# Performance work log

Hardware: AMD Instinct MI355X
Metric: run time of the kernel (lower is better)

## Reference

```python
import jax, jax.numpy as jnp
import numpy as np

N = 8192
D_IN = 3
D_K = 128
HID = 256
N_RES = 2
N_TRI = 2730
N_EDGE = 2048
EPS = float(jnp.finfo(jnp.float32).eps)  # torch RMSNorm default eps=None -> finfo eps


def setup_inputs() -> dict:
    key = jax.random.key(0)
    ks = jax.random.split(key, 16)
    std = 0.02
    inp = {
        "edge_features": jax.random.normal(ks[0], (N, D_IN), dtype=jnp.float32),
        "edge_ids": jax.random.randint(ks[1], (N,), 0, N_EDGE),
        "triangle_ids": jax.random.randint(ks[2], (N,), 0, N_TRI),
        # projections (stored as [in, out]; equivalent to torch Linear)
        "Wq": jax.random.normal(ks[3], (D_IN, D_K), dtype=jnp.float32) * std,
        "bq": jnp.zeros((D_K,), jnp.float32),
        "Wk": jax.random.normal(ks[4], (D_IN, D_K), dtype=jnp.float32) * std,
        "bk": jnp.zeros((D_K,), jnp.float32),
        "Wv": jax.random.normal(ks[5], (D_IN, D_K), dtype=jnp.float32) * std,
        "bv": jnp.zeros((D_K,), jnp.float32),
        # attention MLP: Linear(d_k, hid) -> N_RES ResBlocks -> Linear(hid, 1)
        "W0": jax.random.normal(ks[6], (D_K, HID), dtype=jnp.float32) * std,
        "b0": jnp.zeros((HID,), jnp.float32),
        "rms_w": jnp.ones((N_RES, HID), jnp.float32),
        "Wres": jax.random.normal(ks[7], (N_RES, HID, HID), dtype=jnp.float32) * std,
        "bres": jnp.zeros((N_RES, HID), jnp.float32),
        "Wout": jax.random.normal(ks[8], (HID, 1), dtype=jnp.float32) * std,
        "bout": jnp.zeros((1,), jnp.float32),
    }
    return inp


def _rmsnorm(x, g):
    ms = jnp.mean(x * x, axis=-1, keepdims=True)
    return x * jax.lax.rsqrt(ms + EPS) * g


def reference(edge_features, edge_ids, triangle_ids,
              Wq, bq, Wk, bk, Wv, bv,
              W0, b0, rms_w, Wres, bres, Wout, bout):
    q = edge_features @ Wq + bq          # [N, d_k]
    k = edge_features @ Wk + bk
    v = edge_features @ Wv + bv
    scores = (q @ k.T) / jnp.sqrt(jnp.float32(D_K))   # [N, N]
    mask = triangle_ids[:, None] == triangle_ids[None, :]
    scores = jnp.where(mask, scores, -jnp.inf)
    attn = jax.nn.softmax(scores, axis=1)             # every row has diag True
    attended = attn @ v                                # [N, d_k]
    # MLP with ResBlocks
    h = attended @ W0 + b0                             # [N, hid]
    for i in range(N_RES):
        h = h + jax.nn.relu(_rmsnorm(h, rms_w[i]) @ Wres[i] + bres[i])
    logits = (h @ Wout + bout)[:, 0]                   # [N]
    # scatter_softmax over edge_ids (dim=0)
    seg_max = jax.ops.segment_max(logits, edge_ids, num_segments=N_EDGE)
    ex = jnp.exp(logits - seg_max[edge_ids])
    seg_sum = jax.ops.segment_sum(ex, edge_ids, num_segments=N_EDGE)
    weights = ex / seg_sum[edge_ids]
    return weights
```

## Files before the change

kernel.cpp:

```cpp
#include <hip/hip_runtime.h>
#include <math.h>

#define N 8192
#define D_IN 3
#define D_K 128
#define HID 256
#define N_RES 2
#define N_TRI 2730
#define N_EDGE 2048
#define EPS 1.1920929e-07f

typedef unsigned short u16;
typedef float f32x4 __attribute__((ext_vector_type(4)));
typedef short s16x8 __attribute__((ext_vector_type(8)));

#define OFF_ATTB     0
#define OFF_LOGITS   2097152
#define OFF_TRIOFF   (OFF_LOGITS + 32768)
#define OFF_TRICNT   (OFF_TRIOFF + 11008)
#define OFF_MEMT     (OFF_TRICNT + 11008)
#define OFF_EOFF     (OFF_MEMT + 32768)
#define OFF_ECNT     (OFF_EOFF + 8192)
#define OFF_MEME     (OFF_ECNT + 8192)
#define OFF_WPK      (OFF_MEME + 32768)

__device__ __forceinline__ u16 f2bf(float f) {
    unsigned int u = __float_as_uint(f);
    unsigned int r = (u + 0x7fffu + ((u >> 16) & 1u)) >> 16;
    return (u16)r;
}

__global__ __launch_bounds__(1024) void k_prep(
        const int* __restrict__ tri, const int* __restrict__ eids,
        int* __restrict__ tri_off, int* __restrict__ tri_cnt, int* __restrict__ mem_t,
        int* __restrict__ e_off, int* __restrict__ e_cnt, int* __restrict__ mem_e) {
    __shared__ int sa[4096], sb[4096];
    __shared__ int ea[2048], eb[2048];
    const int t = threadIdx.x;
    for (int i = t; i < 4096; i += 1024) sa[i] = 0;
    for (int i = t; i < 2048; i += 1024) ea[i] = 0;
    __syncthreads();
    for (int n = t; n < N; n += 1024) {
        atomicAdd(&sa[tri[n]], 1);
        atomicAdd(&ea[eids[n]], 1);
    }
    __syncthreads();
    int *src = sa, *dst = sb;
    for (int off = 1; off < 4096; off <<= 1) {
        for (int i = t; i < 4096; i += 1024) {
            int v = src[i];
            if (i >= off) v += src[i - off];
            dst[i] = v;
        }
        __syncthreads();
        int* tmp = src; src = dst; dst = tmp;
    }
    int *es = ea, *ed = eb;
    for (int off = 1; off < 2048; off <<= 1) {
        for (int i = t; i < 2048; i += 1024) {
            int v = es[i];
            if (i >= off) v += es[i - off];
            ed[i] = v;
        }
        __syncthreads();
        int* tmp = es; es = ed; ed = tmp;
    }
    for (int i = t; i < N_TRI; i += 1024) {
        int excl = i ? src[i - 1] : 0;
        tri_off[i] = excl;
        tri_cnt[i] = src[i] - excl;
        dst[i] = excl;
    }
    for (int i = t; i < N_EDGE; i += 1024) {
        int excl = i ? es[i - 1] : 0;
        e_off[i] = excl;
        e_cnt[i] = es[i] - excl;
        ed[i] = excl;
    }
    __syncthreads();
    for (int n = t; n < N; n += 1024) {
        int p = atomicAdd(&dst[tri[n]], 1);
        mem_t[p] = n;
        int q = atomicAdd(&ed[eids[n]], 1);
        mem_e[q] = n;
    }
}

__global__ __launch_bounds__(256) void k_pack(
        const float* __restrict__ W0, const float* __restrict__ Wres,
        u16* __restrict__ Wpk) {
    int tid = blockIdx.x * 256 + threadIdx.x;
    int tile = tid >> 6, lane = tid & 63;
    int q = lane >> 4, c = lane & 15;
    u16 tmp[8];
    int dst;
    if (tile < 64) {
        int nt = tile >> 2, kt = tile & 3;
        int k0 = kt * 32 + q * 8, n = nt * 16 + c;
        dst = (tile * 64 + lane) * 8;
        #pragma unroll
        for (int j = 0; j < 8; ++j) tmp[j] = f2bf(W0[(k0 + j) * HID + n]);
    } else {
        int t2 = tile - 64;
        int r = t2 >> 7, tl = t2 & 127;
        int nt = tl >> 3, kt = tl & 7;
        int k0 = kt * 32 + q * 8, n = nt * 16 + c;
        dst = 32768 + r * 65536 + (tl * 64 + lane) * 8;
        const float* W = Wres + r * 65536;
        #pragma unroll
        for (int j = 0; j < 8; ++j) tmp[j] = f2bf(W[(k0 + j) * HID + n]);
    }
    *(s16x8*)&Wpk[dst] = *(s16x8*)tmp;
}

__global__ __launch_bounds__(256) void k_attn(
        const float* __restrict__ ef, const int* __restrict__ tri,
        const float* __restrict__ Wq, const float* __restrict__ bq,
        const float* __restrict__ Wk, const float* __restrict__ bk,
        const float* __restrict__ Wv, const float* __restrict__ bv,
        const int* __restrict__ tri_offset, const int* __restrict__ tri_count,
        const int* __restrict__ members, u16* __restrict__ att) {
    int wave = threadIdx.x >> 6;
    int lane = threadIdx.x & 63;
    int row = blockIdx.x * 4 + wave;
    int d0 = lane * 2, d1 = lane * 2 + 1;

    float e0 = ef[row * 3 + 0], e1 = ef[row * 3 + 1], e2 = ef[row * 3 + 2];
    float qa = bq[d0] + e0 * Wq[d0] + e1 * Wq[D_K + d0] + e2 * Wq[2 * D_K + d0];
    float qb = bq[d1] + e0 * Wq[d1] + e1 * Wq[D_K + d1] + e2 * Wq[2 * D_K + d1];

    int t = tri[row];
    int off = tri_offset[t], cnt = tri_count[t];
    const float scale = 0.08838834764831845f;

    float m = -INFINITY, l = 0.f, acca = 0.f, accb = 0.f;
    for (int ii = 0; ii < cnt; ++ii) {
        int j = members[off + ii];
        float f0 = ef[j * 3 + 0], f1 = ef[j * 3 + 1], f2 = ef[j * 3 + 2];
        float ka = bk[d0] + f0 * Wk[d0] + f1 * Wk[D_K + d0] + f2 * Wk[2 * D_K + d0];
        float kb = bk[d1] + f0 * Wk[d1] + f1 * Wk[D_K + d1] + f2 * Wk[2 * D_K + d1];
        float p = qa * ka + qb * kb;
        #pragma unroll
        for (int o = 32; o > 0; o >>= 1) p += __shfl_xor(p, o);
        float s = p * scale;
        float va = bv[d0] + f0 * Wv[d0] + f1 * Wv[D_K + d0] + f2 * Wv[2 * D_K + d0];
        float vb = bv[d1] + f0 * Wv[d1] + f1 * Wv[D_K + d1] + f2 * Wv[2 * D_K + d1];
        float mn = fmaxf(m, s);
        float sc = expf(m - mn);
        float w  = expf(s - mn);
        l    = l * sc + w;
        acca = acca * sc + w * va;
        accb = accb * sc + w * vb;
        m = mn;
    }
    att[row * D_K + d0] = f2bf(acca / l);
    att[row * D_K + d1] = f2bf(accb / l);
}

__global__ __launch_bounds__(256) void k_mlp(
        const u16* __restrict__ att,
        const float* __restrict__ b0, const float* __restrict__ rms_w,
        const float* __restrict__ bres, const float* __restrict__ Wout,
        const float* __restrict__ bout, const u16* __restrict__ Wpk,
        float* __restrict__ logits) {
    __shared__ u16 X[16][264];
    __shared__ float red[4][16];
    const int tid = threadIdx.x;
    const int w = tid >> 6, lane = tid & 63;
    const int q = lane >> 4, c = lane & 15;
    const int base = blockIdx.x * 16;
    const int colb = w * 64 + c;

    {
        int r = tid >> 4, kk = (tid & 15) * 8;
        *(s16x8*)&X[r][kk] = *(const s16x8*)&att[(base + r) * D_K + kk];
    }
    __syncthreads();

    const s16x8* Bp = (const s16x8*)Wpk;

    float h[4][4];
    f32x4 acc[4];
    const f32x4 zero = {0.f, 0.f, 0.f, 0.f};

    #pragma unroll
    for (int nt = 0; nt < 4; ++nt) acc[nt] = zero;
    for (int kt = 0; kt < 4; ++kt) {
        s16x8 a = *(const s16x8*)&X[c][kt * 32 + q * 8];
        #pragma unroll
        for (int nt = 0; nt < 4; ++nt) {
            s16x8 b = Bp[((w * 4 + nt) * 4 + kt) * 64 + lane];
            acc[nt] = __builtin_amdgcn_mfma_f32_16x16x32_bf16(a, b, acc[nt], 0, 0, 0);
        }
    }
    #pragma unroll
    for (int nt = 0; nt < 4; ++nt) {
        float bb = b0[colb + nt * 16];
        #pragma unroll
        for (int rg = 0; rg < 4; ++rg) h[nt][rg] = acc[nt][rg] + bb;
    }

    for (int ir = 0; ir < N_RES; ++ir) {
        float part[4];
        #pragma unroll
        for (int rg = 0; rg < 4; ++rg) {
            part[rg] = h[0][rg] * h[0][rg] + h[1][rg] * h[1][rg]
                     + h[2][rg] * h[2][rg] + h[3][rg] * h[3][rg];
            #pragma unroll
            for (int o = 1; o < 16; o <<= 1) part[rg] += __shfl_xor(part[rg], o);
        }
        if (c == 0) {
            #pragma unroll
            for (int rg = 0; rg < 4; ++rg) red[w][q * 4 + rg] = part[rg];
        }
        __syncthreads();
        float sc[4];
        #pragma unroll
        for (int rg = 0; rg < 4; ++rg) {
            int rr = q * 4 + rg;
            float ms = (red[0][rr] + red[1][rr] + red[2][rr] + red[3][rr]) * (1.f / HID);
            sc[rg] = rsqrtf(ms + EPS);
        }
        #pragma unroll
        for (int nt = 0; nt < 4; ++nt) {
            float gg = rms_w[ir * HID + colb + nt * 16];
            #pragma unroll
            for (int rg = 0; rg < 4; ++rg) {
                X[q * 4 + rg][colb + nt * 16] = f2bf(h[nt][rg] * sc[rg] * gg);
            }
        }
        __syncthreads();

        const s16x8* Br = Bp + 4096 + ir * 8192;
        #pragma unroll
        for (int nt = 0; nt < 4; ++nt) acc[nt] = zero;
        for (int kt = 0; kt < 8; ++kt) {
            s16x8 a = *(const s16x8*)&X[c][kt * 32 + q * 8];
            #pragma unroll
            for (int nt = 0; nt < 4; ++nt) {
                s16x8 b = Br[((w * 4 + nt) * 8 + kt) * 64 + lane];
                acc[nt] = __builtin_amdgcn_mfma_f32_16x16x32_bf16(a, b, acc[nt], 0, 0, 0);
            }
        }
        #pragma unroll
        for (int nt = 0; nt < 4; ++nt) {
            float bb = bres[ir * HID + colb + nt * 16];
            #pragma unroll
            for (int rg = 0; rg < 4; ++rg) h[nt][rg] += fmaxf(acc[nt][rg] + bb, 0.f);
        }
    }

    {
        float wo[4];
        #pragma unroll
        for (int nt = 0; nt < 4; ++nt) wo[nt] = Wout[colb + nt * 16];
        float part[4];
        #pragma unroll
        for (int rg = 0; rg < 4; ++rg) {
            part[rg] = h[0][rg] * wo[0] + h[1][rg] * wo[1]
                     + h[2][rg] * wo[2] + h[3][rg] * wo[3];
            #pragma unroll
            for (int o = 1; o < 16; o <<= 1) part[rg] += __shfl_xor(part[rg], o);
        }
        if (c == 0) {
            #pragma unroll
            for (int rg = 0; rg < 4; ++rg) red[w][q * 4 + rg] = part[rg];
        }
        __syncthreads();
        if (tid < 16)
            logits[base + tid] = red[0][tid] + red[1][tid] + red[2][tid] + red[3][tid] + bout[0];
    }
}

__global__ __launch_bounds__(256) void k_segsoft(
        const float* __restrict__ logits, const int* __restrict__ e_off,
        const int* __restrict__ e_cnt, const int* __restrict__ mem_e,
        float* __restrict__ out) {
    int e = (blockIdx.x * 256 + threadIdx.x) >> 6;
    int lane = threadIdx.x & 63;
    int off = e_off[e], cnt = e_cnt[e];
    float mx = -INFINITY;
    for (int i = lane; i < cnt; i += 64) mx = fmaxf(mx, logits[mem_e[off + i]]);
    #pragma unroll
    for (int o = 32; o > 0; o >>= 1) mx = fmaxf(mx, __shfl_xor(mx, o));
    float s = 0.f;
    for (int i = lane; i < cnt; i += 64) s += expf(logits[mem_e[off + i]] - mx);
    #pragma unroll
    for (int o = 32; o > 0; o >>= 1) s += __shfl_xor(s, o);
    float inv = 1.f / s;
    for (int i = lane; i < cnt; i += 64) {
        int m = mem_e[off + i];
        out[m] = expf(logits[m] - mx) * inv;
    }
}

extern "C" void kernel_launch(void* const* d_in, const int* in_sizes, int n_in,
                              void* d_out, int out_size, void* d_ws, size_t ws_size,
                              hipStream_t stream) {
    const float* ef   = (const float*)d_in[0];
    const int*   eids = (const int*)d_in[1];
    const int*   tri  = (const int*)d_in[2];
    const float* Wq = (const float*)d_in[3];
    const float* bq = (const float*)d_in[4];
    const float* Wk = (const float*)d_in[5];
    const float* bk = (const float*)d_in[6];
    const float* Wv = (const float*)d_in[7];
    const float* bv = (const float*)d_in[8];
    const float* W0 = (const float*)d_in[9];
    const float* b0 = (const float*)d_in[10];
    const float* rms_w = (const float*)d_in[11];
    const float* Wres  = (const float*)d_in[12];
    const float* bres  = (const float*)d_in[13];
    const float* Wout  = (const float*)d_in[14];
    const float* bout  = (const float*)d_in[15];
    float* out = (float*)d_out;

    char* ws = (char*)d_ws;
    u16*   attb    = (u16*)(ws + OFF_ATTB);
    float* logits  = (float*)(ws + OFF_LOGITS);
    int*   tri_off = (int*)(ws + OFF_TRIOFF);
    int*   tri_cnt = (int*)(ws + OFF_TRICNT);
    int*   mem_t   = (int*)(ws + OFF_MEMT);
    int*   e_off   = (int*)(ws + OFF_EOFF);
    int*   e_cnt   = (int*)(ws + OFF_ECNT);
    int*   mem_e   = (int*)(ws + OFF_MEME);
    u16*   Wpk     = (u16*)(ws + OFF_WPK);

    hipLaunchKernelGGL(k_prep, dim3(1), dim3(1024), 0, stream,
                       tri, eids, tri_off, tri_cnt, mem_t, e_off, e_cnt, mem_e);
    hipLaunchKernelGGL(k_pack, dim3(80), dim3(256), 0, stream, W0, Wres, Wpk);
    hipLaunchKernelGGL(k_attn, dim3(N / 4), dim3(256), 0, stream,
                       ef, tri, Wq, bq, Wk, bk, Wv, bv, tri_off, tri_cnt, mem_t, attb);
    hipLaunchKernelGGL(k_mlp, dim3(N / 16), dim3(256), 0, stream,
                       attb, b0, rms_w, bres, Wout, bout, Wpk, logits);
    hipLaunchKernelGGL(k_segsoft, dim3(N_EDGE / 4), dim3(256), 0, stream,
                       logits, e_off, e_cnt, mem_e, out);
}
```

Measured before the change: 128.5 us.

## Fuse attention into MLP kernel, merge prep with weight packing, use wave-scan

Merges weight packing into the setup kernel as extra blocks. The single-block Hillis-Steele scans are replaced by a shuffle-based wave scan with fewer barriers. The attention step now runs inside the MLP kernel: each of 8 waves computes two rows, writes bf16 results straight into shared memory, and gathers member features once per 64-member chunk through shuffles. This removes two launches, the global attended buffer round-trip, and repeated scattered global loads, at the cost of halving per-wave MFMA columns and adding block-wide serialization on the attention loop.

```diff
diff --git a/kernel.cpp b/kernel.cpp
--- a/kernel.cpp
+++ b/kernel.cpp
@@ -11,190 +11,216 @@
 #define EPS 1.1920929e-07f
 
 typedef unsigned short u16;
+typedef unsigned int u32;
 typedef float f32x4 __attribute__((ext_vector_type(4)));
 typedef short s16x8 __attribute__((ext_vector_type(8)));
 
-#define OFF_ATTB     0
-#define OFF_LOGITS   2097152
-#define OFF_TRIOFF   (OFF_LOGITS + 32768)
-#define OFF_TRICNT   (OFF_TRIOFF + 11008)
-#define OFF_MEMT     (OFF_TRICNT + 11008)
-#define OFF_EOFF     (OFF_MEMT + 32768)
-#define OFF_ECNT     (OFF_EOFF + 8192)
-#define OFF_MEME     (OFF_ECNT + 8192)
-#define OFF_WPK      (OFF_MEME + 32768)
+#define OFF_LOGITS   0
+#define OFF_TRIOFF   32768
+#define OFF_TRICNT   43776
+#define OFF_MEMT     54784
+#define OFF_EOFF     87552
+#define OFF_ECNT     95744
+#define OFF_MEME     103936
+#define OFF_WPK      136704
 
 __device__ __forceinline__ u16 f2bf(float f) {
-    unsigned int u = __float_as_uint(f);
-    unsigned int r = (u + 0x7fffu + ((u >> 16) & 1u)) >> 16;
+    u32 u = __float_as_uint(f);
+    u32 r = (u + 0x7fffu + ((u >> 16) & 1u)) >> 16;
     return (u16)r;
 }
-
-__global__ __launch_bounds__(1024) void k_prep(
+__device__ __forceinline__ u32 pack2bf(float a, float b) {
+    return (u32)f2bf(a) | ((u32)f2bf(b) << 16);
+}
+
+__global__ __launch_bounds__(1024) void k_setup(
         const int* __restrict__ tri, const int* __restrict__ eids,
+        const float* __restrict__ W0, const float* __restrict__ Wres,
         int* __restrict__ tri_off, int* __restrict__ tri_cnt, int* __restrict__ mem_t,
-        int* __restrict__ e_off, int* __restrict__ e_cnt, int* __restrict__ mem_e) {
-    __shared__ int sa[4096], sb[4096];
-    __shared__ int ea[2048], eb[2048];
-    const int t = threadIdx.x;
-    for (int i = t; i < 4096; i += 1024) sa[i] = 0;
-    for (int i = t; i < 2048; i += 1024) ea[i] = 0;
+        int* __restrict__ e_off, int* __restrict__ e_cnt, int* __restrict__ mem_e,
+        u16* __restrict__ Wpk) {
+    if (blockIdx.x != 0) {
+        int tg = (blockIdx.x - 1) * 1024 + threadIdx.x;
+        int tile = tg >> 6, lane = tg & 63;
+        int q = lane >> 4, c = lane & 15;
+        u16 tmp[8];
+        int dst;
+        if (tile < 64) {
+            int nt = tile >> 2, kt = tile & 3;
+            int k0 = kt * 32 + q * 8, n = nt * 16 + c;
+            dst = (tile * 64 + lane) * 8;
+            #pragma unroll
+            for (int j = 0; j < 8; ++j) tmp[j] = f2bf(W0[(k0 + j) * HID + n]);
+        } else {
+            int t2 = tile - 64;
+            int r = t2 >> 7, tl = t2 & 127;
+            int nt = tl >> 3, kt = tl & 7;
+            int k0 = kt * 32 + q * 8, n = nt * 16 + c;
+            dst = 32768 + r * 65536 + (tl * 64 + lane) * 8;
+            const float* W = Wres + r * 65536;
+            #pragma unroll
+            for (int j = 0; j < 8; ++j) tmp[j] = f2bf(W[(k0 + j) * HID + n]);
+        }
+        *(s16x8*)&Wpk[dst] = *(s16x8*)tmp;
+        return;
+    }
+    __shared__ int sc[4096];
+    __shared__ int ec[2048];
+    __shared__ int wp[16];
+    const int t = threadIdx.x, lane = t & 63, wid = t >> 6;
+    for (int i = t; i < 4096; i += 1024) sc[i] = 0;
+    for (int i = t; i < 2048; i += 1024) ec[i] = 0;
     __syncthreads();
     for (int n = t; n < N; n += 1024) {
-        atomicAdd(&sa[tri[n]], 1);
-        atomicAdd(&ea[eids[n]], 1);
-    }
-    __syncthreads();
-    int *src = sa, *dst = sb;
-    for (int off = 1; off < 4096; off <<= 1) {
-        for (int i = t; i < 4096; i += 1024) {
-            int v = src[i];
-            if (i >= off) v += src[i - off];
-            dst[i] = v;
-        }
-        __syncthreads();
-        int* tmp = src; src = dst; dst = tmp;
-    }
-    int *es = ea, *ed = eb;
-    for (int off = 1; off < 2048; off <<= 1) {
-        for (int i = t; i < 2048; i += 1024) {
-            int v = es[i];
-            if (i >= off) v += es[i - off];
-            ed[i] = v;
-        }
-        __syncthreads();
-        int* tmp = es; es = ed; ed = tmp;
-    }
-    for (int i = t; i < N_TRI; i += 1024) {
-        int excl = i ? src[i - 1] : 0;
-        tri_off[i] = excl;
-        tri_cnt[i] = src[i] - excl;
-        dst[i] = excl;
-    }
-    for (int i = t; i < N_EDGE; i += 1024) {
-        int excl = i ? es[i - 1] : 0;
-        e_off[i] = excl;
-        e_cnt[i] = es[i] - excl;
-        ed[i] = excl;
+        atomicAdd(&sc[tri[n]], 1);
+        atomicAdd(&ec[eids[n]], 1);
+    }
+    __syncthreads();
+    int a0 = sc[t*4], a1 = sc[t*4+1], a2 = sc[t*4+2], a3 = sc[t*4+3];
+    int c0 = a0, c1 = c0 + a1, c2 = c1 + a2, c3 = c2 + a3;
+    int ts = c3;
+    #pragma unroll
+    for (int o = 1; o < 64; o <<= 1) { int u = __shfl_up(ts, o); if (lane >= o) ts += u; }
+    if (lane == 63) wp[wid] = ts;
+    __syncthreads();
+    if (wid == 0) {
+        int v = (lane < 16) ? wp[lane] : 0;
+        #pragma unroll
+        for (int o = 1; o < 16; o <<= 1) { int u = __shfl_up(v, o); if (lane >= o) v += u; }
+        if (lane < 16) wp[lane] = v;
+    }
+    __syncthreads();
+    {
+        int wexcl = wid ? wp[wid - 1] : 0;
+        int texcl = wexcl + ts - c3;
+        int o0 = texcl, o1 = texcl + c0, o2 = texcl + c1, o3 = texcl + c2;
+        if (t*4+0 < N_TRI) { tri_off[t*4+0] = o0; tri_cnt[t*4+0] = a0; }
+        if (t*4+1 < N_TRI) { tri_off[t*4+1] = o1; tri_cnt[t*4+1] = a1; }
+        if (t*4+2 < N_TRI) { tri_off[t*4+2] = o2; tri_cnt[t*4+2] = a2; }
+        if (t*4+3 < N_TRI) { tri_off[t*4+3] = o3; tri_cnt[t*4+3] = a3; }
+        sc[t*4+0] = o0; sc[t*4+1] = o1; sc[t*4+2] = o2; sc[t*4+3] = o3;
+    }
+    __syncthreads();
+    int ea0 = ec[t*2], ea1 = ec[t*2+1];
+    int f0 = ea0, f1 = f0 + ea1;
+    int es = f1;
+    #pragma unroll
+    for (int o = 1; o < 64; o <<= 1) { int u = __shfl_up(es, o); if (lane >= o) es += u; }
+    if (lane == 63) wp[wid] = es;
+    __syncthreads();
+    if (wid == 0) {
+        int v = (lane < 16) ? wp[lane] : 0;
+        #pragma unroll
+        for (int o = 1; o < 16; o <<= 1) { int u = __shfl_up(v, o); if (lane >= o) v += u; }
+        if (lane < 16) wp[lane] = v;
+    }
+    __syncthreads();
+    {
+        int wexcl = wid ? wp[wid - 1] : 0;
+        int texcl = wexcl + es - f1;
+        int eo0 = texcl, eo1 = texcl + f0;
+        e_off[t*2+0] = eo0; e_cnt[t*2+0] = ea0;
+        e_off[t*2+1] = eo1; e_cnt[t*2+1] = ea1;
+        ec[t*2+0] = eo0; ec[t*2+1] = eo1;
     }
     __syncthreads();
     for (int n = t; n < N; n += 1024) {
-        int p = atomicAdd(&dst[tri[n]], 1);
+        int p = atomicAdd(&sc[tri[n]], 1);
         mem_t[p] = n;
-        int q = atomicAdd(&ed[eids[n]], 1);
-        mem_e[q] = n;
-    }
-}
-
-__global__ __launch_bounds__(256) void k_pack(
-        const float* __restrict__ W0, const float* __restrict__ Wres,
-        u16* __restrict__ Wpk) {
-    int tid = blockIdx.x * 256 + threadIdx.x;
-    int tile = tid >> 6, lane = tid & 63;
-    int q = lane >> 4, c = lane & 15;
-    u16 tmp[8];
-    int dst;
-    if (tile < 64) {
-        int nt = tile >> 2, kt = tile & 3;
-        int k0 = kt * 32 + q * 8, n = nt * 16 + c;
-        dst = (tile * 64 + lane) * 8;
-        #pragma unroll
-        for (int j = 0; j < 8; ++j) tmp[j] = f2bf(W0[(k0 + j) * HID + n]);
-    } else {
-        int t2 = tile - 64;
-        int r = t2 >> 7, tl = t2 & 127;
-        int nt = tl >> 3, kt = tl & 7;
-        int k0 = kt * 32 + q * 8, n = nt * 16 + c;
-        dst = 32768 + r * 65536 + (tl * 64 + lane) * 8;
-        const float* W = Wres + r * 65536;
-        #pragma unroll
-        for (int j = 0; j < 8; ++j) tmp[j] = f2bf(W[(k0 + j) * HID + n]);
-    }
-    *(s16x8*)&Wpk[dst] = *(s16x8*)tmp;
-}
-
-__global__ __launch_bounds__(256) void k_attn(
+        int q2 = atomicAdd(&ec[eids[n]], 1);
+        mem_e[q2] = n;
+    }
+}
+
+__global__ __launch_bounds__(512) void k_fused(
         const float* __restrict__ ef, const int* __restrict__ tri,
         const float* __restrict__ Wq, const float* __restrict__ bq,
         const float* __restrict__ Wk, const float* __restrict__ bk,
         const float* __restrict__ Wv, const float* __restrict__ bv,
-        const int* __restrict__ tri_offset, const int* __restrict__ tri_count,
-        const int* __restrict__ members, u16* __restrict__ att) {
-    int wave = threadIdx.x >> 6;
-    int lane = threadIdx.x & 63;
-    int row = blockIdx.x * 4 + wave;
-    int d0 = lane * 2, d1 = lane * 2 + 1;
-
-    float e0 = ef[row * 3 + 0], e1 = ef[row * 3 + 1], e2 = ef[row * 3 + 2];
-    float qa = bq[d0] + e0 * Wq[d0] + e1 * Wq[D_K + d0] + e2 * Wq[2 * D_K + d0];
-    float qb = bq[d1] + e0 * Wq[d1] + e1 * Wq[D_K + d1] + e2 * Wq[2 * D_K + d1];
-
-    int t = tri[row];
-    int off = tri_offset[t], cnt = tri_count[t];
-    const float scale = 0.08838834764831845f;
-
-    float m = -INFINITY, l = 0.f, acca = 0.f, accb = 0.f;
-    for (int ii = 0; ii < cnt; ++ii) {
-        int j = members[off + ii];
-        float f0 = ef[j * 3 + 0], f1 = ef[j * 3 + 1], f2 = ef[j * 3 + 2];
-        float ka = bk[d0] + f0 * Wk[d0] + f1 * Wk[D_K + d0] + f2 * Wk[2 * D_K + d0];
-        float kb = bk[d1] + f0 * Wk[d1] + f1 * Wk[D_K + d1] + f2 * Wk[2 * D_K + d1];
-        float p = qa * ka + qb * kb;
-        #pragma unroll
-        for (int o = 32; o > 0; o >>= 1) p += __shfl_xor(p, o);
-        float s = p * scale;
-        float va = bv[d0] + f0 * Wv[d0] + f1 * Wv[D_K + d0] + f2 * Wv[2 * D_K + d0];
-        float vb = bv[d1] + f0 * Wv[d1] + f1 * Wv[D_K + d1] + f2 * Wv[2 * D_K + d1];
-        float mn = fmaxf(m, s);
-        float sc = expf(m - mn);
-        float w  = expf(s - mn);
-        l    = l * sc + w;
-        acca = acca * sc + w * va;
-        accb = accb * sc + w * vb;
-        m = mn;
-    }
-    att[row * D_K + d0] = f2bf(acca / l);
-    att[row * D_K + d1] = f2bf(accb / l);
-}
-
-__global__ __launch_bounds__(256) void k_mlp(
-        const u16* __restrict__ att,
+        const int* __restrict__ tri_off, const int* __restrict__ tri_cnt,
+        const int* __restrict__ mem_t,
         const float* __restrict__ b0, const float* __restrict__ rms_w,
         const float* __restrict__ bres, const float* __restrict__ Wout,
         const float* __restrict__ bout, const u16* __restrict__ Wpk,
         float* __restrict__ logits) {
     __shared__ u16 X[16][264];
-    __shared__ float red[4][16];
+    __shared__ float red[8][16];
     const int tid = threadIdx.x;
     const int w = tid >> 6, lane = tid & 63;
     const int q = lane >> 4, c = lane & 15;
     const int base = blockIdx.x * 16;
-    const int colb = w * 64 + c;
+    const int colb = w * 32 + c;
 
     {
-        int r = tid >> 4, kk = (tid & 15) * 8;
-        *(s16x8*)&X[r][kk] = *(const s16x8*)&att[(base + r) * D_K + kk];
+        const int d0 = lane * 2, d1 = d0 + 1;
+        float wq0a = Wq[d0], wq1a = Wq[D_K + d0], wq2a = Wq[2*D_K + d0], bqa = bq[d0];
+        float wq0b = Wq[d1], wq1b = Wq[D_K + d1], wq2b = Wq[2*D_K + d1], bqb = bq[d1];
+        float wk0a = Wk[d0], wk1a = Wk[D_K + d0], wk2a = Wk[2*D_K + d0], bka = bk[d0];
+        float wk0b = Wk[d1], wk1b = Wk[D_K + d1], wk2b = Wk[2*D_K + d1], bkb = bk[d1];
+        float wv0a = Wv[d0], wv1a = Wv[D_K + d0], wv2a = Wv[2*D_K + d0], bva = bv[d0];
+        float wv0b = Wv[d1], wv1b = Wv[D_K + d1], wv2b = Wv[2*D_K + d1], bvb = bv[d1];
+        const float scale = 0.08838834764831845f;
+
+        #pragma unroll
+        for (int rr = 0; rr < 2; ++rr) {
+            int lrow = 2 * w + rr;
+            int row = base + lrow;
+            float e0 = ef[row*3+0], e1 = ef[row*3+1], e2 = ef[row*3+2];
+            float qa = bqa + e0*wq0a + e1*wq1a + e2*wq2a;
+            float qb = bqb + e0*wq0b + e1*wq1b + e2*wq2b;
+            int tt = tri[row];
+            int off = tri_off[tt], cnt = tri_cnt[tt];
+            float m = -INFINITY, l = 0.f, acca = 0.f, accb = 0.f;
+            for (int bs = 0; bs < cnt; bs += 64) {
+                int nn = cnt - bs; if (nn > 64) nn = 64;
+                float g0 = 0.f, g1 = 0.f, g2 = 0.f;
+                if (lane < nn) {
+                    int j = mem_t[off + bs + lane];
+                    g0 = ef[j*3+0]; g1 = ef[j*3+1]; g2 = ef[j*3+2];
+                }
+                for (int ii = 0; ii < nn; ++ii) {
+                    float h0 = __shfl(g0, ii), h1 = __shfl(g1, ii), h2 = __shfl(g2, ii);
+                    float ka = bka + h0*wk0a + h1*wk1a + h2*wk2a;
+                    float kb = bkb + h0*wk0b + h1*wk1b + h2*wk2b;
+                    float p = qa * ka + qb * kb;
+                    #pragma unroll
+                    for (int o = 32; o > 0; o >>= 1) p += __shfl_xor(p, o);
+                    float s = p * scale;
+                    float va = bva + h0*wv0a + h1*wv1a + h2*wv2a;
+                    float vb = bvb + h0*wv0b + h1*wv1b + h2*wv2b;
+                    float mn = fmaxf(m, s);
+                    float rs = expf(m - mn);
+                    float ws = expf(s - mn);
+                    l    = l * rs + ws;
+                    acca = acca * rs + ws * va;
+                    accb = accb * rs + ws * vb;
+                    m = mn;
+                }
+            }
+            float inv = 1.f / l;
+            *(u32*)&X[lrow][d0] = pack2bf(acca * inv, accb * inv);
+        }
     }
     __syncthreads();
 
     const s16x8* Bp = (const s16x8*)Wpk;
-
-    float h[4][4];
-    f32x4 acc[4];
+    float h[2][4];
+    f32x4 acc[2];
     const f32x4 zero = {0.f, 0.f, 0.f, 0.f};
 
     #pragma unroll
-    for (int nt = 0; nt < 4; ++nt) acc[nt] = zero;
+    for (int nt = 0; nt < 2; ++nt) acc[nt] = zero;
+    #pragma unroll
     for (int kt = 0; kt < 4; ++kt) {
         s16x8 a = *(const s16x8*)&X[c][kt * 32 + q * 8];
         #pragma unroll
-        for (int nt = 0; nt < 4; ++nt) {
-            s16x8 b = Bp[((w * 4 + nt) * 4 + kt) * 64 + lane];
+        for (int nt = 0; nt < 2; ++nt) {
+            s16x8 b = Bp[((w * 2 + nt) * 4 + kt) * 64 + lane];
             acc[nt] = __builtin_amdgcn_mfma_f32_16x16x32_bf16(a, b, acc[nt], 0, 0, 0);
         }
     }
     #pragma unroll
-    for (int nt = 0; nt < 4; ++nt) {
+    for (int nt = 0; nt < 2; ++nt) {
         float bb = b0[colb + nt * 16];
         #pragma unroll
         for (int rg = 0; rg < 4; ++rg) h[nt][rg] = acc[nt][rg] + bb;
@@ -204,8 +230,7 @@
         float part[4];
         #pragma unroll
         for (int rg = 0; rg < 4; ++rg) {
-            part[rg] = h[0][rg] * h[0][rg] + h[1][rg] * h[1][rg]
-                     + h[2][rg] * h[2][rg] + h[3][rg] * h[3][rg];
+            part[rg] = h[0][rg] * h[0][rg] + h[1][rg] * h[1][rg];
             #pragma unroll
             for (int o = 1; o < 16; o <<= 1) part[rg] += __shfl_xor(part[rg], o);
         }
@@ -214,36 +239,37 @@
             for (int rg = 0; rg < 4; ++rg) red[w][q * 4 + rg] = part[rg];
         }
         __syncthreads();
-        float sc[4];
+        float sc4[4];
         #pragma unroll
         for (int rg = 0; rg < 4; ++rg) {
             int rr = q * 4 + rg;
-            float ms = (red[0][rr] + red[1][rr] + red[2][rr] + red[3][rr]) * (1.f / HID);
-            sc[rg] = rsqrtf(ms + EPS);
-        }
-        #pragma unroll
-        for (int nt = 0; nt < 4; ++nt) {
+            float ms = (red[0][rr] + red[1][rr] + red[2][rr] + red[3][rr]
+                      + red[4][rr] + red[5][rr] + red[6][rr] + red[7][rr]) * (1.f / HID);
+            sc4[rg] = rsqrtf(ms + EPS);
+        }
+        #pragma unroll
+        for (int nt = 0; nt < 2; ++nt) {
             float gg = rms_w[ir * HID + colb + nt * 16];
             #pragma unroll
-            for (int rg = 0; rg < 4; ++rg) {
-                X[q * 4 + rg][colb + nt * 16] = f2bf(h[nt][rg] * sc[rg] * gg);
-            }
+            for (int rg = 0; rg < 4; ++rg)
+                X[q * 4 + rg][colb + nt * 16] = f2bf(h[nt][rg] * sc4[rg] * gg);
         }
         __syncthreads();
 
         const s16x8* Br = Bp + 4096 + ir * 8192;
         #pragma unroll
-        for (int nt = 0; nt < 4; ++nt) acc[nt] = zero;
+        for (int nt = 0; nt < 2; ++nt) acc[nt] = zero;
+        #pragma unroll
         for (int kt = 0; kt < 8; ++kt) {
             s16x8 a = *(const s16x8*)&X[c][kt * 32 + q * 8];
             #pragma unroll
-            for (int nt = 0; nt < 4; ++nt) {
-                s16x8 b = Br[((w * 4 + nt) * 8 + kt) * 64 + lane];
+            for (int nt = 0; nt < 2; ++nt) {
+                s16x8 b = Br[((w * 2 + nt) * 8 + kt) * 64 + lane];
                 acc[nt] = __builtin_amdgcn_mfma_f32_16x16x32_bf16(a, b, acc[nt], 0, 0, 0);
             }
         }
         #pragma unroll
-        for (int nt = 0; nt < 4; ++nt) {
+        for (int nt = 0; nt < 2; ++nt) {
             float bb = bres[ir * HID + colb + nt * 16];
             #pragma unroll
             for (int rg = 0; rg < 4; ++rg) h[nt][rg] += fmaxf(acc[nt][rg] + bb, 0.f);
@@ -251,14 +277,11 @@
     }
 
     {
-        float wo[4];
-        #pragma unroll
-        for (int nt = 0; nt < 4; ++nt) wo[nt] = Wout[colb + nt * 16];
+        float wo0 = Wout[colb], wo1 = Wout[colb + 16];
         float part[4];
         #pragma unroll
         for (int rg = 0; rg < 4; ++rg) {
-            part[rg] = h[0][rg] * wo[0] + h[1][rg] * wo[1]
-                     + h[2][rg] * wo[2] + h[3][rg] * wo[3];
+            part[rg] = h[0][rg] * wo0 + h[1][rg] * wo1;
             #pragma unroll
             for (int o = 1; o < 16; o <<= 1) part[rg] += __shfl_xor(part[rg], o);
         }
@@ -267,8 +290,12 @@
             for (int rg = 0; rg < 4; ++rg) red[w][q * 4 + rg] = part[rg];
         }
         __syncthreads();
-        if (tid < 16)
-            logits[base + tid] = red[0][tid] + red[1][tid] + red[2][tid] + red[3][tid] + bout[0];
+        if (tid < 16) {
+            float s = bout[0];
+            #pragma unroll
+            for (int w2 = 0; w2 < 8; ++w2) s += red[w2][tid];
+            logits[base + tid] = s;
+        }
     }
 }
 
@@ -316,7 +343,6 @@
     float* out = (float*)d_out;
 
     char* ws = (char*)d_ws;
-    u16*   attb    = (u16*)(ws + OFF_ATTB);
     float* logits  = (float*)(ws + OFF_LOGITS);
     int*   tri_off = (int*)(ws + OFF_TRIOFF);
     int*   tri_cnt = (int*)(ws + OFF_TRICNT);
@@ -326,13 +352,13 @@
     int*   mem_e   = (int*)(ws + OFF_MEME);
     u16*   Wpk     = (u16*)(ws + OFF_WPK);
 
-    hipLaunchKernelGGL(k_prep, dim3(1), dim3(1024), 0, stream,
-                       tri, eids, tri_off, tri_cnt, mem_t, e_off, e_cnt, mem_e);
-    hipLaunchKernelGGL(k_pack, dim3(80), dim3(256), 0, stream, W0, Wres, Wpk);
-    hipLaunchKernelGGL(k_attn, dim3(N / 4), dim3(256), 0, stream,
-                       ef, tri, Wq, bq, Wk, bk, Wv, bv, tri_off, tri_cnt, mem_t, attb);
-    hipLaunchKernelGGL(k_mlp, dim3(N / 16), dim3(256), 0, stream,
-                       attb, b0, rms_w, bres, Wout, bout, Wpk, logits);
+    hipLaunchKernelGGL(k_setup, dim3(21), dim3(1024), 0, stream,
+                       tri, eids, W0, Wres,
+                       tri_off, tri_cnt, mem_t, e_off, e_cnt, mem_e, Wpk);
+    hipLaunchKernelGGL(k_fused, dim3(N / 16), dim3(512), 0, stream,
+                       ef, tri, Wq, bq, Wk, bk, Wv, bv,
+                       tri_off, tri_cnt, mem_t,
+                       b0, rms_w, bres, Wout, bout, Wpk, logits);
     hipLaunchKernelGGL(k_segsoft, dim3(N_EDGE / 4), dim3(256), 0, stream,
                        logits, e_off, e_cnt, mem_e, out);
 }
```

Result: faster. 117.8 us, median of 2 (-8.4%).
